# Optimization experiments

Hardware: AMD Instinct MI355X
Metric: run time of the kernel (lower is better)

## Reference

```python
import jax, jax.numpy as jnp
import numpy as np

NMS_SIGMA = 2.0
MASK_THRESH = 0.5
N = 500
H = W = 256
NUM_CLS = 80


def setup_inputs() -> dict:
    key = jax.random.key(0)
    k1, k2, k3 = jax.random.split(key, 3)
    mask_preds = jax.random.uniform(k1, (N, H, W), dtype=jnp.float32)
    cate_scores = jax.random.uniform(k2, (N,), dtype=jnp.float32)
    cate_labels = jax.random.randint(k3, (N,), 0, NUM_CLS, dtype=jnp.int32)
    return {"mask_preds": mask_preds, "cate_scores": cate_scores, "cate_labels": cate_labels}


def reference(mask_preds, cate_scores, cate_labels):
    n = mask_preds.shape[0]
    # binarize masks (SOLOv2 inference: seg_masks = seg_preds > mask_thresh)
    seg_masks = (mask_preds > MASK_THRESH).astype(mask_preds.dtype)  # [N,H,W]
    sum_masks = seg_masks.sum(axis=(1, 2))                           # [N]
    # mask scoring: average soft score inside the binary mask
    seg_scores = (mask_preds * seg_masks).sum(axis=(1, 2)) / jnp.maximum(sum_masks, 1.0)
    scores = cate_scores * seg_scores                                # [N]
    # sort descending by score (matrix-NMS assumes sorted order)
    order = jnp.argsort(-scores)
    scores = scores[order]
    labels = cate_labels[order]
    flat = seg_masks[order].reshape(n, -1)                           # [N,HW]
    sums = sum_masks[order]
    # pairwise mask IoU, upper-triangular (j suppressed by i<j)
    inter = flat @ flat.T                                            # [N,N]
    union = sums[:, None] + sums[None, :] - inter
    iou = jnp.triu(inter / jnp.maximum(union, 1.0), k=1)
    label_match = jnp.triu((labels[:, None] == labels[None, :]).astype(iou.dtype), k=1)
    decay_iou = iou * label_match                                    # [N,N]
    # gaussian matrix-NMS decay
    compensate_iou = decay_iou.max(axis=0)                           # [N]
    decay_matrix = jnp.exp(-NMS_SIGMA * (decay_iou ** 2 - compensate_iou[:, None] ** 2))
    coeff = decay_matrix.min(axis=0)                                 # [N]
    updated_scores = scores * coeff
    return updated_scores
```

## Files before the change

kernel.cpp:

```cpp
#include <hip/hip_runtime.h>
#include <cstdint>

typedef unsigned long long u64;

#define THRESH 0.5f
#define SIGMA 2.0f
#define MAXN 512

__device__ __forceinline__ bool better(float sa, int a, float sb, int b) {
    return (sa > sb) || (sa == sb && a < b);
}

__device__ __forceinline__ float fscore(
    const double* __restrict__ pssum, const int* __restrict__ pcnt,
    const float* __restrict__ cate, int idx, float* __restrict__ sumOut)
{
    const double S = ((pssum[4*idx] + pssum[4*idx+1]) + pssum[4*idx+2]) + pssum[4*idx+3];
    const int C = ((pcnt[4*idx] + pcnt[4*idx+1]) + pcnt[4*idx+2]) + pcnt[4*idx+3];
    *sumOut = (float)C;
    return cate[idx] * (float)(S / (double)(C > 1 ? C : 1));
}

__global__ __launch_bounds__(256) void k_pack(
    const float* __restrict__ preds, u64* __restrict__ packed,
    double* __restrict__ pssum, int* __restrict__ pcnt,
    unsigned* __restrict__ compU, int HW)
{
    const int task = blockIdx.x;
    const int tid = threadIdx.x;
    if (task == 0) {
        for (int t = tid; t < MAXN; t += 256) compU[t] = 0u;
    }
    const int i = task >> 2, sub = task & 3;
    const int seg = HW >> 2;
    const float* src = preds + (size_t)i * HW + (size_t)sub * seg;
    u64* dst = packed + (size_t)i * (HW >> 6) + (size_t)sub * (seg >> 6);
    const int wave = tid >> 6, lane = tid & 63;
    double ssum = 0.0;
    int cnt = 0;
    const int iters = seg >> 12;
    for (int k = 0; k < iters; ++k) {
        const int base = (k << 12) + (wave << 10) + (lane << 2);
        const float4 v0 = *reinterpret_cast<const float4*>(src + base);
        const float4 v1 = *reinterpret_cast<const float4*>(src + base + 256);
        const float4 v2 = *reinterpret_cast<const float4*>(src + base + 512);
        const float4 v3 = *reinterpret_cast<const float4*>(src + base + 768);
        #pragma unroll
        for (int q = 0; q < 4; ++q) {
            const float4 v = (q == 0) ? v0 : (q == 1) ? v1 : (q == 2) ? v2 : v3;
            const bool b0 = v.x > THRESH, b1 = v.y > THRESH, b2 = v.z > THRESH, b3 = v.w > THRESH;
            const u64 m0 = __ballot(b0);
            const u64 m1 = __ballot(b1);
            const u64 m2 = __ballot(b2);
            const u64 m3 = __ballot(b3);
            if (lane < 4) {
                const u64 m = (lane == 0) ? m0 : (lane == 1) ? m1 : (lane == 2) ? m2 : m3;
                dst[(k << 6) + (wave << 4) + (q << 2) + lane] = m;
            }
            cnt += (int)b0 + (int)b1 + (int)b2 + (int)b3;
            ssum += (b0 ? (double)v.x : 0.0) + (b1 ? (double)v.y : 0.0)
                  + (b2 ? (double)v.z : 0.0) + (b3 ? (double)v.w : 0.0);
        }
    }
    for (int off = 32; off > 0; off >>= 1) {
        ssum += __shfl_down(ssum, off);
        cnt  += __shfl_down(cnt, off);
    }
    __shared__ double ls[4];
    __shared__ int lc[4];
    if (lane == 0) { ls[wave] = ssum; lc[wave] = cnt; }
    __syncthreads();
    if (tid == 0) {
        pssum[task] = ls[0] + ls[1] + ls[2] + ls[3];
        pcnt[task]  = lc[0] + lc[1] + lc[2] + lc[3];
    }
}

__global__ __launch_bounds__(256) void k_pairs(
    const u64* __restrict__ packed,
    const double* __restrict__ pssum, const int* __restrict__ pcnt,
    const float* __restrict__ cate, const int* __restrict__ labels,
    unsigned* __restrict__ inter, unsigned* __restrict__ compU,
    int N, int WORDS)
{
    const int wid = (blockIdx.x << 2) + (threadIdx.x >> 6);
    const int lane = threadIdx.x & 63;
    const int nw = gridDim.x << 2;
    const int NN = N * N;
    int i = wid / N;
    int j = wid - i * N;
    for (int p = wid; p < NN; p += nw) {
        if (j > i && labels[i] == labels[j]) {
            const u64* A = packed + (size_t)i * WORDS;
            const u64* B = packed + (size_t)j * WORDS;
            unsigned acc = 0;
            const int iters = WORDS >> 7;
            #pragma unroll 2
            for (int k = 0; k < iters; ++k) {
                const int idx = (k << 7) + (lane << 1);
                const ulonglong2 a = *reinterpret_cast<const ulonglong2*>(A + idx);
                const ulonglong2 b = *reinterpret_cast<const ulonglong2*>(B + idx);
                acc += (unsigned)__popcll(a.x & b.x) + (unsigned)__popcll(a.y & b.y);
            }
            #pragma unroll
            for (int off = 32; off > 0; off >>= 1) acc += __shfl_down(acc, off);
            if (lane == 0) {
                inter[(size_t)i * N + j] = acc;
                float smi, smj;
                const float si = fscore(pssum, pcnt, cate, i, &smi);
                const float sj = fscore(pssum, pcnt, cate, j, &smj);
                const int w = better(si, i, sj, j) ? j : i;
                const float un = (smi + smj) - (float)acc;
                const float iou = (float)acc / fmaxf(un, 1.0f);
                atomicMax(&compU[w], __float_as_uint(iou));
            }
        }
        j += nw;
        while (j >= N) { j -= N; ++i; }
    }
}

__global__ __launch_bounds__(256) void k_final(
    const unsigned* __restrict__ inter,
    const double* __restrict__ pssum, const int* __restrict__ pcnt,
    const float* __restrict__ cate, const int* __restrict__ labels,
    const unsigned* __restrict__ compU, float* __restrict__ out, int N)
{
    __shared__ float s_score[MAXN];
    __shared__ float s_sum[MAXN];
    __shared__ int s_label[MAXN];
    const int tid = threadIdx.x;
    for (int idx = tid; idx < N; idx += 256) {
        float sm;
        s_score[idx] = fscore(pssum, pcnt, cate, idx, &sm);
        s_sum[idx] = sm;
        s_label[idx] = labels[idx];
    }
    __syncthreads();

    const int bI = blockIdx.x;
    const float sb = s_score[bI], sub = s_sum[bI];
    const int lb = s_label[bI];
    float m = -3.0e38f;
    int r = 0;
    for (int a = tid; a < N; a += 256) {
        const bool bet = (a != bI) && better(s_score[a], a, sb, bI);
        r += (int)bet;
        float d = 0.0f;
        if (bet && s_label[a] == lb) {
            const int lo = a < bI ? a : bI, hi = a < bI ? bI : a;
            const float in = (float)inter[(size_t)lo * N + hi];
            const float un = s_sum[a] + sub - in;
            d = in / fmaxf(un, 1.0f);
        }
        const float ca = __uint_as_float(compU[a]);
        m = fmaxf(m, d * d - ca * ca);
    }
    for (int off = 32; off > 0; off >>= 1) {
        m = fmaxf(m, __shfl_down(m, off));
        r += __shfl_down(r, off);
    }
    __shared__ float lm[4];
    __shared__ int lr[4];
    const int wave = tid >> 6, lane = tid & 63;
    if (lane == 0) { lm[wave] = m; lr[wave] = r; }
    __syncthreads();
    if (tid == 0) {
        const float mm = fmaxf(fmaxf(lm[0], lm[1]), fmaxf(lm[2], lm[3]));
        const int rank = lr[0] + lr[1] + lr[2] + lr[3];
        out[rank] = sb * expf(-SIGMA * mm);
    }
}

extern "C" void kernel_launch(void* const* d_in, const int* in_sizes, int n_in,
                              void* d_out, int out_size, void* d_ws, size_t ws_size,
                              hipStream_t stream)
{
    const float* preds  = (const float*)d_in[0];
    const float* cate   = (const float*)d_in[1];
    const int*   labels = (const int*)d_in[2];
    float* out = (float*)d_out;

    const int N = in_sizes[1];
    const int HW = in_sizes[0] / N;
    const int WORDS = HW >> 6;

    char* ws = (char*)d_ws;
    size_t off = 0;
    auto take = [&](size_t bytes) -> void* {
        void* p = ws + off;
        off = (off + bytes + 255) & ~(size_t)255;
        return p;
    };
    u64*      packed = (u64*)     take((size_t)N * WORDS * sizeof(u64));
    double*   pssum  = (double*)  take((size_t)N * 4 * sizeof(double));
    int*      pcnt   = (int*)     take((size_t)N * 4 * sizeof(int));
    unsigned* compU  = (unsigned*)take((size_t)MAXN * sizeof(unsigned));
    unsigned* inter  = (unsigned*)take((size_t)N * N * sizeof(unsigned));
    (void)ws_size; (void)n_in; (void)out_size;

    k_pack<<<N * 4, 256, 0, stream>>>(preds, packed, pssum, pcnt, compU, HW);

    k_pairs<<<1024, 256, 0, stream>>>(packed, pssum, pcnt, cate, labels,
                                      inter, compU, N, WORDS);

    k_final<<<N, 256, 0, stream>>>(inter, pssum, pcnt, cate, labels, compU, out, N);
}
```

Before: 223.8 us.

## Fuse pack, pairwise and final kernels into one cooperative kernel with grid syncs

Merges the three kernels into a single cooperative launch of 1024 blocks, with grid-wide syncs between the bit-packing, pairwise intersection and final decay phases. The pack phase becomes a grid-stride loop over the 2000 tasks, and the final phase runs only on the first N blocks. This removes two kernel launch gaps and their tails. In exchange it adds grid barriers, reduces pack-phase parallelism to the co-resident grid, and needs all 1024 blocks to fit at once under launch bounds of (256,4).

```diff
diff --git a/kernel.cpp b/kernel.cpp
--- a/kernel.cpp
+++ b/kernel.cpp
@@ -1,11 +1,14 @@
 #include <hip/hip_runtime.h>
+#include <hip/hip_cooperative_groups.h>
 #include <cstdint>
 
+namespace cg = cooperative_groups;
 typedef unsigned long long u64;
 
 #define THRESH 0.5f
 #define SIGMA 2.0f
 #define MAXN 512
+#define GRID 1024
 
 __device__ __forceinline__ bool better(float sa, int a, float sb, int b) {
     return (sa > sb) || (sa == sb && a < b);
@@ -21,115 +24,117 @@
     return cate[idx] * (float)(S / (double)(C > 1 ? C : 1));
 }
 
-__global__ __launch_bounds__(256) void k_pack(
-    const float* __restrict__ preds, u64* __restrict__ packed,
+__global__ __launch_bounds__(256, 4) void k_fused(
+    const float* __restrict__ preds, const float* __restrict__ cate,
+    const int* __restrict__ labels, u64* __restrict__ packed,
     double* __restrict__ pssum, int* __restrict__ pcnt,
-    unsigned* __restrict__ compU, int HW)
+    unsigned* __restrict__ inter, unsigned* __restrict__ compU,
+    float* __restrict__ out, int N, int HW)
 {
-    const int task = blockIdx.x;
+    cg::grid_group gg = cg::this_grid();
     const int tid = threadIdx.x;
-    if (task == 0) {
-        for (int t = tid; t < MAXN; t += 256) compU[t] = 0u;
-    }
-    const int i = task >> 2, sub = task & 3;
-    const int seg = HW >> 2;
-    const float* src = preds + (size_t)i * HW + (size_t)sub * seg;
-    u64* dst = packed + (size_t)i * (HW >> 6) + (size_t)sub * (seg >> 6);
     const int wave = tid >> 6, lane = tid & 63;
-    double ssum = 0.0;
-    int cnt = 0;
-    const int iters = seg >> 12;
-    for (int k = 0; k < iters; ++k) {
-        const int base = (k << 12) + (wave << 10) + (lane << 2);
-        const float4 v0 = *reinterpret_cast<const float4*>(src + base);
-        const float4 v1 = *reinterpret_cast<const float4*>(src + base + 256);
-        const float4 v2 = *reinterpret_cast<const float4*>(src + base + 512);
-        const float4 v3 = *reinterpret_cast<const float4*>(src + base + 768);
-        #pragma unroll
-        for (int q = 0; q < 4; ++q) {
-            const float4 v = (q == 0) ? v0 : (q == 1) ? v1 : (q == 2) ? v2 : v3;
-            const bool b0 = v.x > THRESH, b1 = v.y > THRESH, b2 = v.z > THRESH, b3 = v.w > THRESH;
-            const u64 m0 = __ballot(b0);
-            const u64 m1 = __ballot(b1);
-            const u64 m2 = __ballot(b2);
-            const u64 m3 = __ballot(b3);
-            if (lane < 4) {
-                const u64 m = (lane == 0) ? m0 : (lane == 1) ? m1 : (lane == 2) ? m2 : m3;
-                dst[(k << 6) + (wave << 4) + (q << 2) + lane] = m;
-            }
-            cnt += (int)b0 + (int)b1 + (int)b2 + (int)b3;
-            ssum += (b0 ? (double)v.x : 0.0) + (b1 ? (double)v.y : 0.0)
-                  + (b2 ? (double)v.z : 0.0) + (b3 ? (double)v.w : 0.0);
-        }
-    }
-    for (int off = 32; off > 0; off >>= 1) {
-        ssum += __shfl_down(ssum, off);
-        cnt  += __shfl_down(cnt, off);
-    }
+    const int WORDS = HW >> 6;
+
     __shared__ double ls[4];
     __shared__ int lc[4];
-    if (lane == 0) { ls[wave] = ssum; lc[wave] = cnt; }
-    __syncthreads();
-    if (tid == 0) {
-        pssum[task] = ls[0] + ls[1] + ls[2] + ls[3];
-        pcnt[task]  = lc[0] + lc[1] + lc[2] + lc[3];
-    }
-}
-
-__global__ __launch_bounds__(256) void k_pairs(
-    const u64* __restrict__ packed,
-    const double* __restrict__ pssum, const int* __restrict__ pcnt,
-    const float* __restrict__ cate, const int* __restrict__ labels,
-    unsigned* __restrict__ inter, unsigned* __restrict__ compU,
-    int N, int WORDS)
-{
-    const int wid = (blockIdx.x << 2) + (threadIdx.x >> 6);
-    const int lane = threadIdx.x & 63;
-    const int nw = gridDim.x << 2;
-    const int NN = N * N;
-    int i = wid / N;
-    int j = wid - i * N;
-    for (int p = wid; p < NN; p += nw) {
-        if (j > i && labels[i] == labels[j]) {
-            const u64* A = packed + (size_t)i * WORDS;
-            const u64* B = packed + (size_t)j * WORDS;
-            unsigned acc = 0;
-            const int iters = WORDS >> 7;
-            #pragma unroll 2
-            for (int k = 0; k < iters; ++k) {
-                const int idx = (k << 7) + (lane << 1);
-                const ulonglong2 a = *reinterpret_cast<const ulonglong2*>(A + idx);
-                const ulonglong2 b = *reinterpret_cast<const ulonglong2*>(B + idx);
-                acc += (unsigned)__popcll(a.x & b.x) + (unsigned)__popcll(a.y & b.y);
-            }
-            #pragma unroll
-            for (int off = 32; off > 0; off >>= 1) acc += __shfl_down(acc, off);
-            if (lane == 0) {
-                inter[(size_t)i * N + j] = acc;
-                float smi, smj;
-                const float si = fscore(pssum, pcnt, cate, i, &smi);
-                const float sj = fscore(pssum, pcnt, cate, j, &smj);
-                const int w = better(si, i, sj, j) ? j : i;
-                const float un = (smi + smj) - (float)acc;
-                const float iou = (float)acc / fmaxf(un, 1.0f);
-                atomicMax(&compU[w], __float_as_uint(iou));
-            }
-        }
-        j += nw;
-        while (j >= N) { j -= N; ++i; }
-    }
-}
-
-__global__ __launch_bounds__(256) void k_final(
-    const unsigned* __restrict__ inter,
-    const double* __restrict__ pssum, const int* __restrict__ pcnt,
-    const float* __restrict__ cate, const int* __restrict__ labels,
-    const unsigned* __restrict__ compU, float* __restrict__ out, int N)
-{
     __shared__ float s_score[MAXN];
     __shared__ float s_sum[MAXN];
     __shared__ int s_label[MAXN];
-    const int tid = threadIdx.x;
+    __shared__ float lm[4];
+    __shared__ int lr[4];
+
+    if (blockIdx.x == 0) {
+        for (int t = tid; t < MAXN; t += 256) compU[t] = 0u;
+    }
+    const int ntask = N * 4;
+    const int seg = HW >> 2;
+    for (int task = blockIdx.x; task < ntask; task += gridDim.x) {
+        const int i = task >> 2, sub = task & 3;
+        const float* src = preds + (size_t)i * HW + (size_t)sub * seg;
+        u64* dst = packed + (size_t)i * WORDS + (size_t)sub * (seg >> 6);
+        double ssum = 0.0;
+        int cnt = 0;
+        const int iters = seg >> 12;
+        for (int k = 0; k < iters; ++k) {
+            const int base = (k << 12) + (wave << 10) + (lane << 2);
+            const float4 v0 = *reinterpret_cast<const float4*>(src + base);
+            const float4 v1 = *reinterpret_cast<const float4*>(src + base + 256);
+            const float4 v2 = *reinterpret_cast<const float4*>(src + base + 512);
+            const float4 v3 = *reinterpret_cast<const float4*>(src + base + 768);
+            #pragma unroll
+            for (int q = 0; q < 4; ++q) {
+                const float4 v = (q == 0) ? v0 : (q == 1) ? v1 : (q == 2) ? v2 : v3;
+                const bool b0 = v.x > THRESH, b1 = v.y > THRESH, b2 = v.z > THRESH, b3 = v.w > THRESH;
+                const u64 m0 = __ballot(b0);
+                const u64 m1 = __ballot(b1);
+                const u64 m2 = __ballot(b2);
+                const u64 m3 = __ballot(b3);
+                if (lane < 4) {
+                    const u64 m = (lane == 0) ? m0 : (lane == 1) ? m1 : (lane == 2) ? m2 : m3;
+                    dst[(k << 6) + (wave << 4) + (q << 2) + lane] = m;
+                }
+                cnt += (int)b0 + (int)b1 + (int)b2 + (int)b3;
+                ssum += (b0 ? (double)v.x : 0.0) + (b1 ? (double)v.y : 0.0)
+                      + (b2 ? (double)v.z : 0.0) + (b3 ? (double)v.w : 0.0);
+            }
+        }
+        for (int off = 32; off > 0; off >>= 1) {
+            ssum += __shfl_down(ssum, off);
+            cnt  += __shfl_down(cnt, off);
+        }
+        if (lane == 0) { ls[wave] = ssum; lc[wave] = cnt; }
+        __syncthreads();
+        if (tid == 0) {
+            pssum[task] = ls[0] + ls[1] + ls[2] + ls[3];
+            pcnt[task]  = lc[0] + lc[1] + lc[2] + lc[3];
+        }
+        __syncthreads();
+    }
+    __threadfence();
+    gg.sync();
+
+    {
+        const int wid = (blockIdx.x << 2) + wave;
+        const int nw = gridDim.x << 2;
+        const int NN = N * N;
+        int i = wid / N;
+        int j = wid - i * N;
+        for (int p = wid; p < NN; p += nw) {
+            if (j > i && labels[i] == labels[j]) {
+                const u64* A = packed + (size_t)i * WORDS;
+                const u64* B = packed + (size_t)j * WORDS;
+                unsigned acc = 0;
+                const int iters = WORDS >> 7;
+                #pragma unroll 2
+                for (int k = 0; k < iters; ++k) {
+                    const int idx = (k << 7) + (lane << 1);
+                    const ulonglong2 a = *reinterpret_cast<const ulonglong2*>(A + idx);
+                    const ulonglong2 b = *reinterpret_cast<const ulonglong2*>(B + idx);
+                    acc += (unsigned)__popcll(a.x & b.x) + (unsigned)__popcll(a.y & b.y);
+                }
+                #pragma unroll
+                for (int off = 32; off > 0; off >>= 1) acc += __shfl_down(acc, off);
+                if (lane == 0) {
+                    inter[(size_t)i * N + j] = acc;
+                    float smi, smj;
+                    const float si = fscore(pssum, pcnt, cate, i, &smi);
+                    const float sj = fscore(pssum, pcnt, cate, j, &smj);
+                    const int w = better(si, i, sj, j) ? j : i;
+                    const float un = (smi + smj) - (float)acc;
+                    const float iou = (float)acc / fmaxf(un, 1.0f);
+                    atomicMax(&compU[w], __float_as_uint(iou));
+                }
+            }
+            j += nw;
+            while (j >= N) { j -= N; ++i; }
+        }
+    }
+    __threadfence();
+    gg.sync();
+
+    const int bI = blockIdx.x;
+    if (bI >= N) return;
     for (int idx = tid; idx < N; idx += 256) {
         float sm;
         s_score[idx] = fscore(pssum, pcnt, cate, idx, &sm);
@@ -138,7 +143,6 @@
     }
     __syncthreads();
 
-    const int bI = blockIdx.x;
     const float sb = s_score[bI], sub = s_sum[bI];
     const int lb = s_label[bI];
     float m = -3.0e38f;
@@ -160,9 +164,6 @@
         m = fmaxf(m, __shfl_down(m, off));
         r += __shfl_down(r, off);
     }
-    __shared__ float lm[4];
-    __shared__ int lr[4];
-    const int wave = tid >> 6, lane = tid & 63;
     if (lane == 0) { lm[wave] = m; lr[wave] = r; }
     __syncthreads();
     if (tid == 0) {
@@ -181,8 +182,8 @@
     const int*   labels = (const int*)d_in[2];
     float* out = (float*)d_out;
 
-    const int N = in_sizes[1];
-    const int HW = in_sizes[0] / N;
+    int N = in_sizes[1];
+    int HW = in_sizes[0] / N;
     const int WORDS = HW >> 6;
 
     char* ws = (char*)d_ws;
@@ -199,10 +200,11 @@
     unsigned* inter  = (unsigned*)take((size_t)N * N * sizeof(unsigned));
     (void)ws_size; (void)n_in; (void)out_size;
 
-    k_pack<<<N * 4, 256, 0, stream>>>(preds, packed, pssum, pcnt, compU, HW);
-
-    k_pairs<<<1024, 256, 0, stream>>>(packed, pssum, pcnt, cate, labels,
-                                      inter, compU, N, WORDS);
-
-    k_final<<<N, 256, 0, stream>>>(inter, pssum, pcnt, cate, labels, compU, out, N);
-}
+    void* args[] = {
+        (void*)&preds, (void*)&cate, (void*)&labels, (void*)&packed,
+        (void*)&pssum, (void*)&pcnt, (void*)&inter, (void*)&compU,
+        (void*)&out, (void*)&N, (void*)&HW
+    };
+    hipLaunchCooperativeKernel((const void*)k_fused, dim3(GRID), dim3(256),
+                               args, 0, stream);
+}
```

New measurement: 607.4 us. 171% more time.
